# Optimization experiments

Measured on AMD Instinct MI355X. Metric: run time of the kernel, lower is better.

The kernel has to match this reference:

```python
import jax, jax.numpy as jnp
import numpy as np

N_NODES = 100000
N_EDGES = 640000
IN_DIM = 64
HID = 128
NUM_GRAPHS = 128
MPNN_STEPS = 3
S2S_STEPS = 3


def setup_inputs() -> dict:
    key = jax.random.key(0)
    ks = jax.random.split(key, 20)
    x = jax.random.normal(ks[0], (N_NODES, IN_DIM), dtype=jnp.float32)
    edge_index = jax.random.randint(ks[1], (2, N_EDGES), 0, N_NODES, dtype=jnp.int32)
    batch = jnp.sort(jax.random.randint(ks[2], (N_NODES,), 0, NUM_GRAPHS, dtype=jnp.int32))
    s = 1.0 / np.sqrt(HID)
    params = {
        # input layer Linear(64 -> 128)
        'W_in': jax.random.normal(ks[3], (HID, IN_DIM), dtype=jnp.float32) * s,
        'b_in': jax.random.normal(ks[4], (HID,), dtype=jnp.float32) * s,
        # MGU parameters (torch.randn init in source)
        'W_f': jax.random.normal(ks[5], (HID, HID), dtype=jnp.float32),
        'U_f': jax.random.normal(ks[6], (HID, HID), dtype=jnp.float32),
        'b_f': jax.random.normal(ks[7], (HID,), dtype=jnp.float32),
        'W_h': jax.random.normal(ks[8], (HID, HID), dtype=jnp.float32),
        'U_h': jax.random.normal(ks[9], (HID, HID), dtype=jnp.float32),
        'b_h': jax.random.normal(ks[10], (HID,), dtype=jnp.float32),
        # Set2Set LSTM: input 2*HID, hidden HID, gate order i,f,g,o
        'lstm_w_ih': jax.random.normal(ks[11], (4 * HID, 2 * HID), dtype=jnp.float32) * s,
        'lstm_w_hh': jax.random.normal(ks[12], (4 * HID, HID), dtype=jnp.float32) * s,
        'lstm_b_ih': jax.random.normal(ks[13], (4 * HID,), dtype=jnp.float32) * s,
        'lstm_b_hh': jax.random.normal(ks[14], (4 * HID,), dtype=jnp.float32) * s,
        # prediction layer Linear(2*HID -> 1)
        'W_pred': jax.random.normal(ks[15], (1, 2 * HID), dtype=jnp.float32) * s,
        'b_pred': jax.random.normal(ks[16], (1,), dtype=jnp.float32) * s,
    }
    return {'x': x, 'edge_index': edge_index, 'batch': batch, **params}


def _mpnn_mgu(h, src, dst, W_f, U_f, b_f, W_h, U_h, b_h):
    # sum-aggregate neighbor messages: m_i = sum_{j->i} h_j
    m = jax.ops.segment_sum(h[src], dst, num_segments=N_NODES)  # [N, H]
    f_t = jax.nn.sigmoid(m @ W_f.T + h @ U_f.T + b_f)
    h_hat = jnp.tanh(m @ W_h.T + (f_t * h) @ U_h.T + b_h)
    return (1.0 - f_t) * h + f_t * h_hat


def _set2set(x, batch, w_ih, w_hh, b_ih, b_hh):
    G, H = NUM_GRAPHS, HID
    q_star = jnp.zeros((G, 2 * H), dtype=x.dtype)
    h_l = jnp.zeros((G, H), dtype=x.dtype)
    c_l = jnp.zeros((G, H), dtype=x.dtype)
    for _ in range(S2S_STEPS):
        gates = q_star @ w_ih.T + h_l @ w_hh.T + b_ih + b_hh  # [G, 4H]
        i, f, g, o = jnp.split(gates, 4, axis=-1)
        c_l = jax.nn.sigmoid(f) * c_l + jax.nn.sigmoid(i) * jnp.tanh(g)
        h_l = jax.nn.sigmoid(o) * jnp.tanh(c_l)
        q = h_l  # [G, H]
        # attention over nodes within each graph segment
        e = jnp.sum(x * q[batch], axis=-1)  # [N]
        e_max = jax.ops.segment_max(e, batch, num_segments=G)
        a_un = jnp.exp(e - e_max[batch])
        denom = jax.ops.segment_sum(a_un, batch, num_segments=G)
        a = a_un / denom[batch]
        r = jax.ops.segment_sum(a[:, None] * x, batch, num_segments=G)  # [G, H]
        q_star = jnp.concatenate([q, r], axis=-1)
    return q_star


def reference(x, edge_index, batch, W_in, b_in, W_f, U_f, b_f, W_h, U_h, b_h,
              lstm_w_ih, lstm_w_hh, lstm_b_ih, lstm_b_hh, W_pred, b_pred):
    h = jax.nn.relu(x @ W_in.T + b_in)  # [N, HID]
    src, dst = edge_index[0], edge_index[1]
    for _ in range(MPNN_STEPS):
        h = _mpnn_mgu(h, src, dst, W_f, U_f, b_f, W_h, U_h, b_h)
    q_star = _set2set(h, batch, lstm_w_ih, lstm_w_hh, lstm_b_ih, lstm_b_hh)  # [G, 2H]
    return q_star @ W_pred.T + b_pred  # [G, 1]
```

## Files before the change

### kernel.cpp

```cpp
#include <hip/hip_runtime.h>
#include <math.h>

#define N_NODES 100000
#define N_EDGES 640000
#define IN_DIM 64
#define HID 128
#define NGRAPH 128

typedef __bf16 bf16x2 __attribute__((ext_vector_type(2)));
typedef __bf16 bf16x4 __attribute__((ext_vector_type(4)));
typedef __bf16 bf16x8 __attribute__((ext_vector_type(8)));
typedef float f32x4 __attribute__((ext_vector_type(4)));

#define LDST 136

__device__ __forceinline__ float sigmoid_f(float z) {
  return __fdividef(1.f, 1.f + __expf(-z));
}
__device__ __forceinline__ float tanh_f(float z) {
  return 1.f - __fdividef(2.f, __expf(2.f * z) + 1.f);
}

__device__ __forceinline__ void fma44(const float4 A[4], const float4 B[4], float acc[4][4]) {
#pragma unroll
  for (int i2 = 0; i2 < 4; ++i2) {
    acc[i2][0] += A[i2].x*B[0].x + A[i2].y*B[1].x + A[i2].z*B[2].x + A[i2].w*B[3].x;
    acc[i2][1] += A[i2].x*B[0].y + A[i2].y*B[1].y + A[i2].z*B[2].y + A[i2].w*B[3].y;
    acc[i2][2] += A[i2].x*B[0].z + A[i2].y*B[1].z + A[i2].z*B[2].z + A[i2].w*B[3].z;
    acc[i2][3] += A[i2].x*B[0].w + A[i2].y*B[1].w + A[i2].z*B[2].w + A[i2].w*B[3].w;
  }
}

__global__ __launch_bounds__(256) void k_input(const float* __restrict__ x,
                                               const float* __restrict__ W,
                                               const float* __restrict__ b,
                                               float* __restrict__ h) {
  __shared__ float wS[64][132];
  __shared__ float xS[32][68];
  int t = threadIdx.x;
  int nb = blockIdx.x * 32;
#pragma unroll
  for (int i = 0; i < 8; ++i) {
    int idx4 = i * 256 + t;
    int j = idx4 >> 4, kq = idx4 & 15;
    float4 v = ((const float4*)W)[j * 16 + kq];
    wS[4*kq+0][j] = v.x; wS[4*kq+1][j] = v.y; wS[4*kq+2][j] = v.z; wS[4*kq+3][j] = v.w;
  }
#pragma unroll
  for (int i = 0; i < 2; ++i) {
    int idx4 = i * 256 + t;
    int n = idx4 >> 4, kq = idx4 & 15;
    float4 v = ((const float4*)x)[(nb + n) * 16 + kq];
    *((float4*)&xS[n][4*kq]) = v;
  }
  __syncthreads();
  int bq = t & 31, a = t >> 5;
  float acc[4][4] = {};
#pragma unroll
  for (int kk4 = 0; kk4 < 16; ++kk4) {
    float4 A[4], B[4];
#pragma unroll
    for (int i2 = 0; i2 < 4; ++i2) A[i2] = *((const float4*)&xS[4*a+i2][4*kk4]);
#pragma unroll
    for (int c = 0; c < 4; ++c) B[c] = *((const float4*)&wS[4*kk4+c][4*bq]);
    fma44(A, B, acc);
  }
  float4 bb = ((const float4*)b)[bq];
  float ba[4] = {bb.x, bb.y, bb.z, bb.w};
#pragma unroll
  for (int i2 = 0; i2 < 4; ++i2) {
    float4 o;
    o.x = fmaxf(acc[i2][0] + ba[0], 0.f);
    o.y = fmaxf(acc[i2][1] + ba[1], 0.f);
    o.z = fmaxf(acc[i2][2] + ba[2], 0.f);
    o.w = fmaxf(acc[i2][3] + ba[3], 0.f);
    ((float4*)h)[(nb + 4*a + i2) * 32 + bq] = o;
  }
}

__global__ __launch_bounds__(256) void k_hist(const int* __restrict__ dst,
                                              int* __restrict__ deg) {
  int e = blockIdx.x * 256 + threadIdx.x;
  if (e < N_EDGES) atomicAdd(&deg[dst[e]], 1);
}

#define SCAN_CHUNK 4096
#define SCAN_NB 25

__global__ __launch_bounds__(256) void k_scan_part(const int* __restrict__ deg,
                                                   int* __restrict__ bsum) {
  __shared__ int red[256];
  int t = threadIdx.x, b = blockIdx.x;
  int base = b * SCAN_CHUNK + t * 16;
  int s = 0;
#pragma unroll
  for (int i = 0; i < 16; ++i) {
    int idx = base + i;
    if (idx < N_NODES) s += deg[idx];
  }
  red[t] = s;
  __syncthreads();
  for (int off = 128; off > 0; off >>= 1) {
    if (t < off) red[t] += red[t + off];
    __syncthreads();
  }
  if (t == 0) bsum[b] = red[0];
}

__global__ void k_scan_mid(const int* __restrict__ bsum, int* __restrict__ boff,
                           int* __restrict__ rowstart) {
  if (threadIdx.x == 0) {
    int run = 0;
    for (int i = 0; i < SCAN_NB; ++i) { boff[i] = run; run += bsum[i]; }
    rowstart[N_NODES] = run;
  }
}

__global__ __launch_bounds__(256) void k_scan_final(const int* __restrict__ deg,
                                                    const int* __restrict__ boff,
                                                    int* __restrict__ rowstart) {
  __shared__ int ts[256];
  int t = threadIdx.x, b = blockIdx.x;
  int base = b * SCAN_CHUNK + t * 16;
  int v[16];
  int s = 0;
#pragma unroll
  for (int i = 0; i < 16; ++i) {
    int idx = base + i;
    v[i] = (idx < N_NODES) ? deg[idx] : 0;
    s += v[i];
  }
  ts[t] = s;
  __syncthreads();
  for (int off = 1; off < 256; off <<= 1) {
    int add = (t >= off) ? ts[t - off] : 0;
    __syncthreads();
    ts[t] += add;
    __syncthreads();
  }
  int run = boff[b] + ts[t] - s;
#pragma unroll
  for (int i = 0; i < 16; ++i) {
    int idx = base + i;
    if (idx < N_NODES) rowstart[idx] = run;
    run += v[i];
  }
}

__global__ __launch_bounds__(256) void k_fill(const int* __restrict__ src,
                                              const int* __restrict__ dst,
                                              int* __restrict__ cursor,
                                              int* __restrict__ srcSorted) {
  int e = blockIdx.x * 256 + threadIdx.x;
  if (e >= N_EDGES) return;
  int d = dst[e];
  int p = atomicAdd(&cursor[d], 1);
  srcSorted[p] = src[e];
}

__global__ __launch_bounds__(256) void k_wsplit(const float* __restrict__ W0,
                                                const float* __restrict__ W1,
                                                const float* __restrict__ W2,
                                                const float* __restrict__ W3,
                                                __bf16* __restrict__ Whi,
                                                __bf16* __restrict__ Wlo) {
  int id = blockIdx.x * 256 + threadIdx.x;
  int mat = id >> 14, idx = id & 16383;
  const float* W = (mat == 0) ? W0 : (mat == 1) ? W1 : (mat == 2) ? W2 : W3;
  float v = W[idx];
  __bf16 hi = (__bf16)v;
  Whi[id] = hi;
  Wlo[id] = (__bf16)(v - (float)hi);
}

__global__ __launch_bounds__(256) void k_gather(const float* __restrict__ h,
                                                const int* __restrict__ rowstart,
                                                const int* __restrict__ srcSorted,
                                                float* __restrict__ m) {
  int node = blockIdx.x * 8 + (threadIdx.x >> 5);
  if (node >= N_NODES) return;
  int li = threadIdx.x & 31;
  int j0 = rowstart[node], j1 = rowstart[node + 1];
  const float4* h4 = (const float4*)h;
  float4 a0 = {0.f, 0.f, 0.f, 0.f}, a1 = {0.f, 0.f, 0.f, 0.f};
  int j = j0;
  for (; j + 1 < j1; j += 2) {
    int s0 = srcSorted[j], s1 = srcSorted[j + 1];
    float4 v0 = h4[s0 * 32 + li];
    float4 v1 = h4[s1 * 32 + li];
    a0.x += v0.x; a0.y += v0.y; a0.z += v0.z; a0.w += v0.w;
    a1.x += v1.x; a1.y += v1.y; a1.z += v1.z; a1.w += v1.w;
  }
  if (j < j1) {
    int s0 = srcSorted[j];
    float4 v0 = h4[s0 * 32 + li];
    a0.x += v0.x; a0.y += v0.y; a0.z += v0.z; a0.w += v0.w;
  }
  float4 o = {a0.x + a1.x, a0.y + a1.y, a0.z + a1.z, a0.w + a1.w};
  ((float4*)m)[node * 32 + li] = o;
}

__global__ __launch_bounds__(256) void k_mgu(float* __restrict__ h,
                                             const float* __restrict__ m,
                                             const __bf16* __restrict__ Whi,
                                             const __bf16* __restrict__ Wlo,
                                             const float* __restrict__ bfp,
                                             const float* __restrict__ bhp) {
  __shared__ __bf16 mHi[64 * LDST], mLo[64 * LDST];
  __shared__ __bf16 hHi[64 * LDST], hLo[64 * LDST];
  const int t = threadIdx.x;
  const int nb = blockIdx.x * 64;

#pragma unroll
  for (int i = 0; i < 8; ++i) {
    int idx4 = i * 256 + t;
    int n = idx4 >> 5, kq = idx4 & 31;
    float4 vm = ((const float4*)m)[(nb + n) * 32 + kq];
    float4 vh = ((const float4*)h)[(nb + n) * 32 + kq];
    bf16x4 mh, ml, hh, hl;
    mh[0] = (__bf16)vm.x; ml[0] = (__bf16)(vm.x - (float)mh[0]);
    mh[1] = (__bf16)vm.y; ml[1] = (__bf16)(vm.y - (float)mh[1]);
    mh[2] = (__bf16)vm.z; ml[2] = (__bf16)(vm.z - (float)mh[2]);
    mh[3] = (__bf16)vm.w; ml[3] = (__bf16)(vm.w - (float)mh[3]);
    hh[0] = (__bf16)vh.x; hl[0] = (__bf16)(vh.x - (float)hh[0]);
    hh[1] = (__bf16)vh.y; hl[1] = (__bf16)(vh.y - (float)hh[1]);
    hh[2] = (__bf16)vh.z; hl[2] = (__bf16)(vh.z - (float)hh[2]);
    hh[3] = (__bf16)vh.w; hl[3] = (__bf16)(vh.w - (float)hh[3]);
    int e0 = n * LDST + 4 * kq;
    *(bf16x4*)&mHi[e0] = mh; *(bf16x4*)&mLo[e0] = ml;
    *(bf16x4*)&hHi[e0] = hh; *(bf16x4*)&hLo[e0] = hl;
  }
  __syncthreads();

  const int w = t >> 6, l = t & 63;
  const int lj = l & 15, q = l >> 4;

  float bfj[2], bhj[2];
#pragma unroll
  for (int ct = 0; ct < 2; ++ct) {
    int j = (2 * w + ct) * 16 + lj;
    bfj[ct] = bfp[j];
    bhj[ct] = bhp[j];
  }

  f32x4 acc[4][2] = {};

#pragma unroll
  for (int kc = 0; kc < 128; kc += 32) {
    bf16x8 bwh[2], bwl[2], buh[2], bul[2];
#pragma unroll
    for (int ct = 0; ct < 2; ++ct) {
      int off = ((2 * w + ct) * 16 + lj) * 128 + kc + q * 8;
      bwh[ct] = *(const bf16x8*)&Whi[off];
      bwl[ct] = *(const bf16x8*)&Wlo[off];
      buh[ct] = *(const bf16x8*)&Whi[16384 + off];
      bul[ct] = *(const bf16x8*)&Wlo[16384 + off];
    }
#pragma unroll
    for (int rt = 0; rt < 4; ++rt) {
      int e0 = (rt * 16 + lj) * LDST + kc + q * 8;
      bf16x8 amh = *(const bf16x8*)&mHi[e0];
      bf16x8 aml = *(const bf16x8*)&mLo[e0];
      bf16x8 ahh = *(const bf16x8*)&hHi[e0];
      bf16x8 ahl = *(const bf16x8*)&hLo[e0];
#pragma unroll
      for (int ct = 0; ct < 2; ++ct) {
        f32x4 a = acc[rt][ct];
        a = __builtin_amdgcn_mfma_f32_16x16x32_bf16(amh, bwh[ct], a, 0, 0, 0);
        a = __builtin_amdgcn_mfma_f32_16x16x32_bf16(amh, bwl[ct], a, 0, 0, 0);
        a = __builtin_amdgcn_mfma_f32_16x16x32_bf16(aml, bwh[ct], a, 0, 0, 0);
        a = __builtin_amdgcn_mfma_f32_16x16x32_bf16(ahh, buh[ct], a, 0, 0, 0);
        a = __builtin_amdgcn_mfma_f32_16x16x32_bf16(ahh, bul[ct], a, 0, 0, 0);
        a = __builtin_amdgcn_mfma_f32_16x16x32_bf16(ahl, buh[ct], a, 0, 0, 0);
        acc[rt][ct] = a;
      }
    }
  }

  __syncthreads();
  float fv[4][2][4], hvv[4][2][4];
#pragma unroll
  for (int rt = 0; rt < 4; ++rt)
#pragma unroll
    for (int ct = 0; ct < 2; ++ct) {
      int j = (2 * w + ct) * 16 + lj;
#pragma unroll
      for (int r = 0; r < 4; ++r) {
        int nl = rt * 16 + q * 4 + r;
        float z = acc[rt][ct][r] + bfj[ct];
        float f = sigmoid_f(z);
        int he = nl * LDST + j;
        float hval = (float)hHi[he] + (float)hLo[he];
        float g = f * hval;
        __bf16 ghi = (__bf16)g;
        hHi[he] = ghi;
        hLo[he] = (__bf16)(g - (float)ghi);
        fv[rt][ct][r] = f;
        hvv[rt][ct][r] = hval;
        acc[rt][ct][r] = 0.f;
      }
    }
  __syncthreads();

#pragma unroll
  for (int kc = 0; kc < 128; kc += 32) {
    bf16x8 bwh[2], bwl[2], buh[2], bul[2];
#pragma unroll
    for (int ct = 0; ct < 2; ++ct) {
      int off = ((2 * w + ct) * 16 + lj) * 128 + kc + q * 8;
      bwh[ct] = *(const bf16x8*)&Whi[2 * 16384 + off];
      bwl[ct] = *(const bf16x8*)&Wlo[2 * 16384 + off];
      buh[ct] = *(const bf16x8*)&Whi[3 * 16384 + off];
      bul[ct] = *(const bf16x8*)&Wlo[3 * 16384 + off];
    }
#pragma unroll
    for (int rt = 0; rt < 4; ++rt) {
      int e0 = (rt * 16 + lj) * LDST + kc + q * 8;
      bf16x8 amh = *(const bf16x8*)&mHi[e0];
      bf16x8 aml = *(const bf16x8*)&mLo[e0];
      bf16x8 agh = *(const bf16x8*)&hHi[e0];
      bf16x8 agl = *(const bf16x8*)&hLo[e0];
#pragma unroll
      for (int ct = 0; ct < 2; ++ct) {
        f32x4 a = acc[rt][ct];
        a = __builtin_amdgcn_mfma_f32_16x16x32_bf16(amh, bwh[ct], a, 0, 0, 0);
        a = __builtin_amdgcn_mfma_f32_16x16x32_bf16(amh, bwl[ct], a, 0, 0, 0);
        a = __builtin_amdgcn_mfma_f32_16x16x32_bf16(aml, bwh[ct], a, 0, 0, 0);
        a = __builtin_amdgcn_mfma_f32_16x16x32_bf16(agh, buh[ct], a, 0, 0, 0);
        a = __builtin_amdgcn_mfma_f32_16x16x32_bf16(agh, bul[ct], a, 0, 0, 0);
        a = __builtin_amdgcn_mfma_f32_16x16x32_bf16(agl, buh[ct], a, 0, 0, 0);
        acc[rt][ct] = a;
      }
    }
  }

#pragma unroll
  for (int rt = 0; rt < 4; ++rt)
#pragma unroll
    for (int ct = 0; ct < 2; ++ct) {
      int j = (2 * w + ct) * 16 + lj;
#pragma unroll
      for (int r = 0; r < 4; ++r) {
        float T = tanh_f(acc[rt][ct][r] + bhj[ct]);
        float f = fv[rt][ct][r];
        float hn = (1.f - f) * hvv[rt][ct][r] + f * T;
        h[(nb + rt * 16 + q * 4 + r) * 128 + j] = hn;
      }
    }
}

__global__ __launch_bounds__(1024) void k_s2s(const float* __restrict__ h,
                                              const int* __restrict__ batch,
                                              const float* __restrict__ w_ih,
                                              const float* __restrict__ w_hh,
                                              const float* __restrict__ b_ih,
                                              const float* __restrict__ b_hh,
                                              const float* __restrict__ Wp,
                                              const float* __restrict__ bp,
                                              float* __restrict__ out) {
  const int g = blockIdx.x, t = threadIdx.x;
  const int w = t >> 6, l = t & 63;
  const int half = l >> 5, li = l & 31;
  const int hw = 2 * w + half;
  __shared__ float qs[256];
  __shared__ float hl[128], cl[128];
  __shared__ float gates[512];
  __shared__ float redM[32], redS[32], scl[32];
  __shared__ float rPart[32][132];
  __shared__ float gInvS;
  __shared__ int bnd[2];

  if (t < 2) {
    int tgt = g + t;
    int lo = 0, hi = N_NODES;
    while (lo < hi) { int mid = (lo + hi) >> 1; if (batch[mid] < tgt) lo = mid + 1; else hi = mid; }
    bnd[t] = lo;
  }
  if (t < 256) qs[t] = 0.f;
  if (t < 128) { hl[t] = 0.f; cl[t] = 0.f; }
  __syncthreads();
  const int s0 = bnd[0], s1 = bnd[1];

  for (int step = 0; step < 3; ++step) {
#pragma unroll 2
    for (int jt = w; jt < 512; jt += 16) {
      const float* wi = w_ih + jt * 256;
      const float* wh = w_hh + jt * 128;
      float s = qs[l] * wi[l] + qs[l+64] * wi[l+64]
              + qs[l+128] * wi[l+128] + qs[l+192] * wi[l+192]
              + hl[l] * wh[l] + hl[l+64] * wh[l+64];
#pragma unroll
      for (int o = 32; o > 0; o >>= 1) s += __shfl_xor(s, o, 64);
      if (l == 0) gates[jt] = s + b_ih[jt] + b_hh[jt];
    }
    __syncthreads();
    if (t < 128) {
      float gi = gates[t], gf = gates[128 + t], gg = gates[256 + t], go = gates[384 + t];
      float c = sigmoid_f(gf) * cl[t] + sigmoid_f(gi) * tanh_f(gg);
      float hh = sigmoid_f(go) * tanh_f(c);
      cl[t] = c;
      hl[t] = hh;
      qs[t] = hh;
    }
    __syncthreads();

    float mw = -INFINITY, sw = 0.f;
    float4 racc = {0.f, 0.f, 0.f, 0.f};
    const float4* h4 = (const float4*)h;
    const float q0 = qs[4*li], q1 = qs[4*li+1], q2 = qs[4*li+2], q3 = qs[4*li+3];
    int n = s0 + hw;
    for (; n + 32 < s1; n += 64) {
      float4 hv0 = h4[n * 32 + li];
      float4 hv1 = h4[(n + 32) * 32 + li];
      float v0 = hv0.x * q0 + hv0.y * q1 + hv0.z * q2 + hv0.w * q3;
      float v1 = hv1.x * q0 + hv1.y * q1 + hv1.z * q2 + hv1.w * q3;
#pragma unroll
      for (int o = 16; o > 0; o >>= 1) {
        v0 += __shfl_xor(v0, o, 64);
        v1 += __shfl_xor(v1, o, 64);
      }
      float nm = fmaxf(mw, fmaxf(v0, v1));
      float sc = __expf(mw - nm);
      float w0 = __expf(v0 - nm);
      float w1 = __expf(v1 - nm);
      sw = sw * sc + w0 + w1;
      racc.x = racc.x * sc + w0 * hv0.x + w1 * hv1.x;
      racc.y = racc.y * sc + w0 * hv0.y + w1 * hv1.y;
      racc.z = racc.z * sc + w0 * hv0.z + w1 * hv1.z;
      racc.w = racc.w * sc + w0 * hv0.w + w1 * hv1.w;
      mw = nm;
    }
    for (; n < s1; n += 32) {
      float4 hv = h4[n * 32 + li];
      float v = hv.x * q0 + hv.y * q1 + hv.z * q2 + hv.w * q3;
#pragma unroll
      for (int o = 16; o > 0; o >>= 1) v += __shfl_xor(v, o, 64);
      float nm = fmaxf(mw, v);
      float sc = __expf(mw - nm);
      float wg = __expf(v - nm);
      sw = sw * sc + wg;
      racc.x = racc.x * sc + wg * hv.x;
      racc.y = racc.y * sc + wg * hv.y;
      racc.z = racc.z * sc + wg * hv.z;
      racc.w = racc.w * sc + wg * hv.w;
      mw = nm;
    }
    if (li == 0) { redM[hw] = mw; redS[hw] = sw; }
    *(float4*)&rPart[hw][4 * li] = racc;
    __syncthreads();
    if (t == 0) {
      float M = -INFINITY;
      for (int i = 0; i < 32; ++i) M = fmaxf(M, redM[i]);
      float S = 0.f;
      for (int i = 0; i < 32; ++i) {
        float s_ = (redM[i] > -INFINITY && M > -INFINITY) ? __expf(redM[i] - M) : 0.f;
        scl[i] = s_;
        S += redS[i] * s_;
      }
      gInvS = (S > 0.f) ? __fdividef(1.f, S) : 0.f;
    }
    __syncthreads();
    if (t < 128) {
      float inv = gInvS;
      float r = 0.f;
#pragma unroll
      for (int i = 0; i < 32; ++i) r += rPart[i][t] * scl[i];
      qs[128 + t] = r * inv;
    }
    __syncthreads();
  }

  __shared__ float pr[256];
  if (t < 256) pr[t] = qs[t] * Wp[t];
  __syncthreads();
  if (t < 128) pr[t] += pr[t + 128];
  __syncthreads();
  if (t < 64) {
    float s = pr[t] + pr[t + 64];
#pragma unroll
    for (int o = 32; o > 0; o >>= 1) s += __shfl_xor(s, o, 64);
    if (t == 0) out[g] = s + bp[0];
  }
}

extern "C" void kernel_launch(void* const* d_in, const int* in_sizes, int n_in,
                              void* d_out, int out_size, void* d_ws, size_t ws_size,
                              hipStream_t stream) {
  const float* x      = (const float*)d_in[0];
  const int*   ei     = (const int*)d_in[1];
  const int*   batch  = (const int*)d_in[2];
  const float* W_in   = (const float*)d_in[3];
  const float* b_in   = (const float*)d_in[4];
  const float* W_f    = (const float*)d_in[5];
  const float* U_f    = (const float*)d_in[6];
  const float* b_f    = (const float*)d_in[7];
  const float* W_h    = (const float*)d_in[8];
  const float* U_h    = (const float*)d_in[9];
  const float* b_h    = (const float*)d_in[10];
  const float* w_ih   = (const float*)d_in[11];
  const float* w_hh   = (const float*)d_in[12];
  const float* b_ih   = (const float*)d_in[13];
  const float* b_hh   = (const float*)d_in[14];
  const float* W_pred = (const float*)d_in[15];
  const float* b_pred = (const float*)d_in[16];
  float* out = (float*)d_out;

  char* ws = (char*)d_ws;
  float* h      = (float*)(ws);
  float* m      = (float*)(ws + 51200000);
  int*   rowstart = (int*)(ws + 103063808);
  int*   srcSorted= (int*)(ws + 103463824);
  int*   bsum   = (int*)  (ws + 106023824);
  int*   boff   = (int*)  (ws + 106023936);
  int*    deg    = (int*)(ws + 102400000);
  int*    cursor = (int*)(ws + 102400000);
  __bf16* Whi    = (__bf16*)(ws + 102400000);
  __bf16* Wlo    = (__bf16*)(ws + 102531072);

  const int* src = ei;
  const int* dst = ei + N_EDGES;

  hipMemsetAsync(deg, 0, N_NODES * 4, stream);
  k_hist<<<(N_EDGES + 255) / 256, 256, 0, stream>>>(dst, deg);
  k_scan_part<<<SCAN_NB, 256, 0, stream>>>(deg, bsum);
  k_scan_mid<<<1, 32, 0, stream>>>(bsum, boff, rowstart);
  k_scan_final<<<SCAN_NB, 256, 0, stream>>>(deg, boff, rowstart);
  hipMemcpyAsync(cursor, rowstart, N_NODES * 4, hipMemcpyDeviceToDevice, stream);
  k_fill<<<(N_EDGES + 255) / 256, 256, 0, stream>>>(src, dst, cursor, srcSorted);

  k_wsplit<<<256, 256, 0, stream>>>(W_f, U_f, W_h, U_h, Whi, Wlo);

  k_input<<<N_NODES / 32, 256, 0, stream>>>(x, W_in, b_in, h);

  for (int step = 0; step < 3; ++step) {
    k_gather<<<(N_NODES + 7) / 8, 256, 0, stream>>>(h, rowstart, srcSorted, m);
    k_mgu<<<(N_NODES + 63) / 64, 256, 0, stream>>>(h, m, Whi, Wlo, b_f, b_h);
  }

  k_s2s<<<NGRAPH, 1024, 0, stream>>>(h, batch, w_ih, w_hh, b_ih, b_hh,
                                     W_pred, b_pred, out);
}
```

Before: 725.1 us.

## Fuse neighbor gather into MGU kernel with ping-pong hidden buffers

```diff
diff --git a/kernel.cpp b/kernel.cpp
--- a/kernel.cpp
+++ b/kernel.cpp
@@ -173,35 +173,10 @@
   Wlo[id] = (__bf16)(v - (float)hi);
 }
 
-__global__ __launch_bounds__(256) void k_gather(const float* __restrict__ h,
-                                                const int* __restrict__ rowstart,
-                                                const int* __restrict__ srcSorted,
-                                                float* __restrict__ m) {
-  int node = blockIdx.x * 8 + (threadIdx.x >> 5);
-  if (node >= N_NODES) return;
-  int li = threadIdx.x & 31;
-  int j0 = rowstart[node], j1 = rowstart[node + 1];
-  const float4* h4 = (const float4*)h;
-  float4 a0 = {0.f, 0.f, 0.f, 0.f}, a1 = {0.f, 0.f, 0.f, 0.f};
-  int j = j0;
-  for (; j + 1 < j1; j += 2) {
-    int s0 = srcSorted[j], s1 = srcSorted[j + 1];
-    float4 v0 = h4[s0 * 32 + li];
-    float4 v1 = h4[s1 * 32 + li];
-    a0.x += v0.x; a0.y += v0.y; a0.z += v0.z; a0.w += v0.w;
-    a1.x += v1.x; a1.y += v1.y; a1.z += v1.z; a1.w += v1.w;
-  }
-  if (j < j1) {
-    int s0 = srcSorted[j];
-    float4 v0 = h4[s0 * 32 + li];
-    a0.x += v0.x; a0.y += v0.y; a0.z += v0.z; a0.w += v0.w;
-  }
-  float4 o = {a0.x + a1.x, a0.y + a1.y, a0.z + a1.z, a0.w + a1.w};
-  ((float4*)m)[node * 32 + li] = o;
-}
-
-__global__ __launch_bounds__(256) void k_mgu(float* __restrict__ h,
-                                             const float* __restrict__ m,
+__global__ __launch_bounds__(256) void k_mgu(float* __restrict__ hdst,
+                                             const float* __restrict__ hsrc,
+                                             const int* __restrict__ rowstart,
+                                             const int* __restrict__ srcSorted,
                                              const __bf16* __restrict__ Whi,
                                              const __bf16* __restrict__ Wlo,
                                              const float* __restrict__ bfp,
@@ -215,20 +190,48 @@
   for (int i = 0; i < 8; ++i) {
     int idx4 = i * 256 + t;
     int n = idx4 >> 5, kq = idx4 & 31;
-    float4 vm = ((const float4*)m)[(nb + n) * 32 + kq];
-    float4 vh = ((const float4*)h)[(nb + n) * 32 + kq];
-    bf16x4 mh, ml, hh, hl;
-    mh[0] = (__bf16)vm.x; ml[0] = (__bf16)(vm.x - (float)mh[0]);
-    mh[1] = (__bf16)vm.y; ml[1] = (__bf16)(vm.y - (float)mh[1]);
-    mh[2] = (__bf16)vm.z; ml[2] = (__bf16)(vm.z - (float)mh[2]);
-    mh[3] = (__bf16)vm.w; ml[3] = (__bf16)(vm.w - (float)mh[3]);
+    float4 vh = ((const float4*)hsrc)[(nb + n) * 32 + kq];
+    bf16x4 hh, hl;
     hh[0] = (__bf16)vh.x; hl[0] = (__bf16)(vh.x - (float)hh[0]);
     hh[1] = (__bf16)vh.y; hl[1] = (__bf16)(vh.y - (float)hh[1]);
     hh[2] = (__bf16)vh.z; hl[2] = (__bf16)(vh.z - (float)hh[2]);
     hh[3] = (__bf16)vh.w; hl[3] = (__bf16)(vh.w - (float)hh[3]);
     int e0 = n * LDST + 4 * kq;
-    *(bf16x4*)&mHi[e0] = mh; *(bf16x4*)&mLo[e0] = ml;
     *(bf16x4*)&hHi[e0] = hh; *(bf16x4*)&hLo[e0] = hl;
+  }
+
+  {
+    const int grp = t >> 5, li = t & 31;
+    const float4* h4 = (const float4*)hsrc;
+#pragma unroll 1
+    for (int c = 0; c < 8; ++c) {
+      int nl = c * 8 + grp;
+      int node = nb + nl;
+      int j0 = 0, j1 = 0;
+      if (node < N_NODES) { j0 = rowstart[node]; j1 = rowstart[node + 1]; }
+      float4 a0 = {0.f, 0.f, 0.f, 0.f}, a1 = {0.f, 0.f, 0.f, 0.f};
+      int j = j0;
+      for (; j + 1 < j1; j += 2) {
+        int s0 = srcSorted[j], s1 = srcSorted[j + 1];
+        float4 v0 = h4[s0 * 32 + li];
+        float4 v1 = h4[s1 * 32 + li];
+        a0.x += v0.x; a0.y += v0.y; a0.z += v0.z; a0.w += v0.w;
+        a1.x += v1.x; a1.y += v1.y; a1.z += v1.z; a1.w += v1.w;
+      }
+      if (j < j1) {
+        int s0 = srcSorted[j];
+        float4 v0 = h4[s0 * 32 + li];
+        a0.x += v0.x; a0.y += v0.y; a0.z += v0.z; a0.w += v0.w;
+      }
+      float4 o = {a0.x + a1.x, a0.y + a1.y, a0.z + a1.z, a0.w + a1.w};
+      bf16x4 mh, ml;
+      mh[0] = (__bf16)o.x; ml[0] = (__bf16)(o.x - (float)mh[0]);
+      mh[1] = (__bf16)o.y; ml[1] = (__bf16)(o.y - (float)mh[1]);
+      mh[2] = (__bf16)o.z; ml[2] = (__bf16)(o.z - (float)mh[2]);
+      mh[3] = (__bf16)o.w; ml[3] = (__bf16)(o.w - (float)mh[3]);
+      int e0 = nl * LDST + 4 * li;
+      *(bf16x4*)&mHi[e0] = mh; *(bf16x4*)&mLo[e0] = ml;
+    }
   }
   __syncthreads();
 
@@ -341,10 +344,11 @@
       int j = (2 * w + ct) * 16 + lj;
 #pragma unroll
       for (int r = 0; r < 4; ++r) {
+        int node = nb + rt * 16 + q * 4 + r;
         float T = tanh_f(acc[rt][ct][r] + bhj[ct]);
         float f = fv[rt][ct][r];
         float hn = (1.f - f) * hvv[rt][ct][r] + f * T;
-        h[(nb + rt * 16 + q * 4 + r) * 128 + j] = hn;
+        if (node < N_NODES) hdst[node * 128 + j] = hn;
       }
     }
 }
@@ -506,8 +510,8 @@
   float* out = (float*)d_out;
 
   char* ws = (char*)d_ws;
-  float* h      = (float*)(ws);
-  float* m      = (float*)(ws + 51200000);
+  float* h0     = (float*)(ws);
+  float* h1     = (float*)(ws + 51200000);
   int*   rowstart = (int*)(ws + 103063808);
   int*   srcSorted= (int*)(ws + 103463824);
   int*   bsum   = (int*)  (ws + 106023824);
@@ -530,13 +534,13 @@
 
   k_wsplit<<<256, 256, 0, stream>>>(W_f, U_f, W_h, U_h, Whi, Wlo);
 
-  k_input<<<N_NODES / 32, 256, 0, stream>>>(x, W_in, b_in, h);
-
-  for (int step = 0; step < 3; ++step) {
-    k_gather<<<(N_NODES + 7) / 8, 256, 0, stream>>>(h, rowstart, srcSorted, m);
-    k_mgu<<<(N_NODES + 63) / 64, 256, 0, stream>>>(h, m, Whi, Wlo, b_f, b_h);
-  }
-
-  k_s2s<<<NGRAPH, 1024, 0, stream>>>(h, batch, w_ih, w_hh, b_ih, b_hh,
+  k_input<<<N_NODES / 32, 256, 0, stream>>>(x, W_in, b_in, h0);
+
+  const int NBLK = (N_NODES + 63) / 64;
+  k_mgu<<<NBLK, 256, 0, stream>>>(h1, h0, rowstart, srcSorted, Whi, Wlo, b_f, b_h);
+  k_mgu<<<NBLK, 256, 0, stream>>>(h0, h1, rowstart, srcSorted, Whi, Wlo, b_f, b_h);
+  k_mgu<<<NBLK, 256, 0, stream>>>(h1, h0, rowstart, srcSorted, Whi, Wlo, b_f, b_h);
+
+  k_s2s<<<NGRAPH, 1024, 0, stream>>>(h1, batch, w_ih, w_hh, b_ih, b_hh,
                                      W_pred, b_pred, out);
 }
```

After: 839.0 us. 1.16x slower.

## Split Set2Set attention across four blocks per graph with last-block LSTM update

Applied to the files above, without the earlier changes.

```diff
diff --git a/kernel.cpp b/kernel.cpp
--- a/kernel.cpp
+++ b/kernel.cpp
@@ -6,6 +6,8 @@
 #define IN_DIM 64
 #define HID 128
 #define NGRAPH 128
+#define SPLIT 4
+#define PSTR 132
 
 typedef __bf16 bf16x2 __attribute__((ext_vector_type(2)));
 typedef __bf16 bf16x4 __attribute__((ext_vector_type(4)));
@@ -349,26 +351,50 @@
     }
 }
 
-__global__ __launch_bounds__(1024) void k_s2s(const float* __restrict__ h,
-                                              const int* __restrict__ batch,
-                                              const float* __restrict__ w_ih,
-                                              const float* __restrict__ w_hh,
-                                              const float* __restrict__ b_ih,
-                                              const float* __restrict__ b_hh,
-                                              const float* __restrict__ Wp,
-                                              const float* __restrict__ bp,
-                                              float* __restrict__ out) {
-  const int g = blockIdx.x, t = threadIdx.x;
+__global__ __launch_bounds__(128) void k_s2s_init(const float* __restrict__ b_ih,
+                                                  const float* __restrict__ b_hh,
+                                                  float* __restrict__ q_buf,
+                                                  float* __restrict__ hc_buf,
+                                                  int* __restrict__ done) {
+  int g = blockIdx.x, t = threadIdx.x;
+  float gi = b_ih[t] + b_hh[t];
+  float gf = b_ih[128 + t] + b_hh[128 + t];
+  float gg = b_ih[256 + t] + b_hh[256 + t];
+  float go = b_ih[384 + t] + b_hh[384 + t];
+  (void)gf;
+  float c = sigmoid_f(gi) * tanh_f(gg);
+  float hh = sigmoid_f(go) * tanh_f(c);
+  q_buf[g * 128 + t] = hh;
+  hc_buf[g * 256 + t] = hh;
+  hc_buf[g * 256 + 128 + t] = c;
+  if (t < 3) done[t * NGRAPH + g] = 0;
+}
+
+__global__ __launch_bounds__(1024, 8) void k_s2s_step(const float* __restrict__ h,
+                                                      const int* __restrict__ batch,
+                                                      float* __restrict__ q_buf,
+                                                      float* __restrict__ hc_buf,
+                                                      float* __restrict__ partials,
+                                                      int* __restrict__ done,
+                                                      const float* __restrict__ w_ih,
+                                                      const float* __restrict__ w_hh,
+                                                      const float* __restrict__ b_ih,
+                                                      const float* __restrict__ b_hh,
+                                                      const float* __restrict__ Wp,
+                                                      const float* __restrict__ bp,
+                                                      float* __restrict__ out,
+                                                      int step) {
+  const int b = blockIdx.x;
+  const int g = b >> 2, p = b & (SPLIT - 1);
+  const int t = threadIdx.x;
   const int w = t >> 6, l = t & 63;
   const int half = l >> 5, li = l & 31;
   const int hw = 2 * w + half;
-  __shared__ float qs[256];
-  __shared__ float hl[128], cl[128];
-  __shared__ float gates[512];
   __shared__ float redM[32], redS[32], scl[32];
   __shared__ float rPart[32][132];
-  __shared__ float gInvS;
+  __shared__ float sMS[2];
   __shared__ int bnd[2];
+  __shared__ int amLast;
 
   if (t < 2) {
     int tgt = g + t;
@@ -376,110 +402,167 @@
     while (lo < hi) { int mid = (lo + hi) >> 1; if (batch[mid] < tgt) lo = mid + 1; else hi = mid; }
     bnd[t] = lo;
   }
-  if (t < 256) qs[t] = 0.f;
-  if (t < 128) { hl[t] = 0.f; cl[t] = 0.f; }
   __syncthreads();
   const int s0 = bnd[0], s1 = bnd[1];
-
-  for (int step = 0; step < 3; ++step) {
-#pragma unroll 2
-    for (int jt = w; jt < 512; jt += 16) {
-      const float* wi = w_ih + jt * 256;
-      const float* wh = w_hh + jt * 128;
-      float s = qs[l] * wi[l] + qs[l+64] * wi[l+64]
-              + qs[l+128] * wi[l+128] + qs[l+192] * wi[l+192]
-              + hl[l] * wh[l] + hl[l+64] * wh[l+64];
+  const int len = s1 - s0;
+  const int ps = s0 + (len * p) / SPLIT;
+  const int pe = s0 + (len * (p + 1)) / SPLIT;
+
+  float4 qv = ((const float4*)(q_buf + g * 128))[li];
+  const float q0 = qv.x, q1 = qv.y, q2 = qv.z, q3 = qv.w;
+
+  float mw = -INFINITY, sw = 0.f;
+  float4 racc = {0.f, 0.f, 0.f, 0.f};
+  const float4* h4 = (const float4*)h;
+  int n = ps + hw;
+  for (; n + 32 < pe; n += 64) {
+    float4 hv0 = h4[n * 32 + li];
+    float4 hv1 = h4[(n + 32) * 32 + li];
+    float v0 = hv0.x * q0 + hv0.y * q1 + hv0.z * q2 + hv0.w * q3;
+    float v1 = hv1.x * q0 + hv1.y * q1 + hv1.z * q2 + hv1.w * q3;
+#pragma unroll
+    for (int o = 16; o > 0; o >>= 1) {
+      v0 += __shfl_xor(v0, o, 64);
+      v1 += __shfl_xor(v1, o, 64);
+    }
+    float nm = fmaxf(mw, fmaxf(v0, v1));
+    float sc = __expf(mw - nm);
+    float w0 = __expf(v0 - nm);
+    float w1 = __expf(v1 - nm);
+    sw = sw * sc + w0 + w1;
+    racc.x = racc.x * sc + w0 * hv0.x + w1 * hv1.x;
+    racc.y = racc.y * sc + w0 * hv0.y + w1 * hv1.y;
+    racc.z = racc.z * sc + w0 * hv0.z + w1 * hv1.z;
+    racc.w = racc.w * sc + w0 * hv0.w + w1 * hv1.w;
+    mw = nm;
+  }
+  for (; n < pe; n += 32) {
+    float4 hv = h4[n * 32 + li];
+    float v = hv.x * q0 + hv.y * q1 + hv.z * q2 + hv.w * q3;
+#pragma unroll
+    for (int o = 16; o > 0; o >>= 1) v += __shfl_xor(v, o, 64);
+    float nm = fmaxf(mw, v);
+    float sc = __expf(mw - nm);
+    float wg = __expf(v - nm);
+    sw = sw * sc + wg;
+    racc.x = racc.x * sc + wg * hv.x;
+    racc.y = racc.y * sc + wg * hv.y;
+    racc.z = racc.z * sc + wg * hv.z;
+    racc.w = racc.w * sc + wg * hv.w;
+    mw = nm;
+  }
+  if (li == 0) { redM[hw] = mw; redS[hw] = sw; }
+  *(float4*)&rPart[hw][4 * li] = racc;
+  __syncthreads();
+  if (t == 0) {
+    float M = -INFINITY;
+    for (int i = 0; i < 32; ++i) M = fmaxf(M, redM[i]);
+    float S = 0.f;
+    for (int i = 0; i < 32; ++i) {
+      float s_ = (redM[i] > -INFINITY && M > -INFINITY) ? __expf(redM[i] - M) : 0.f;
+      scl[i] = s_;
+      S += redS[i] * s_;
+    }
+    sMS[0] = M; sMS[1] = S;
+  }
+  __syncthreads();
+  float* P = partials + (g * SPLIT + p) * PSTR;
+  if (t == 0) { P[0] = sMS[0]; P[1] = sMS[1]; }
+  if (t < 128) {
+    float r = 0.f;
+#pragma unroll
+    for (int i = 0; i < 32; ++i) r += rPart[i][t] * scl[i];
+    P[4 + t] = r;
+  }
+
+  __syncthreads();
+  if (t == 0) {
+    __threadfence();
+    int old = atomicAdd(&done[step * NGRAPH + g], 1);
+    amLast = (old == 3);
+  }
+  __syncthreads();
+  if (!amLast) return;
+  if (t == 0) __threadfence();
+  __syncthreads();
+
+  __shared__ float sc2[SPLIT];
+  __shared__ float qstar[256];
+  __shared__ float hcl[256];
+  __shared__ float gates[512];
+  __shared__ float invS_sh;
+  const float* PP = partials + g * SPLIT * PSTR;
+
+  if (t == 0) {
+    float M = -INFINITY;
+#pragma unroll
+    for (int pp = 0; pp < SPLIT; ++pp) M = fmaxf(M, PP[pp * PSTR]);
+    float S = 0.f;
+#pragma unroll
+    for (int pp = 0; pp < SPLIT; ++pp) {
+      float mp = PP[pp * PSTR];
+      float s_ = (mp > -INFINITY && M > -INFINITY) ? __expf(mp - M) : 0.f;
+      sc2[pp] = s_;
+      S += PP[pp * PSTR + 1] * s_;
+    }
+    invS_sh = (S > 0.f) ? __fdividef(1.f, S) : 0.f;
+  }
+  if (t < 128) {
+    qstar[t] = q_buf[g * 128 + t];
+    hcl[t] = hc_buf[g * 256 + t];
+    hcl[128 + t] = hc_buf[g * 256 + 128 + t];
+  }
+  __syncthreads();
+  if (t < 128) {
+    float r = 0.f;
+#pragma unroll
+    for (int pp = 0; pp < SPLIT; ++pp) r += PP[pp * PSTR + 4 + t] * sc2[pp];
+    qstar[128 + t] = r * invS_sh;
+  }
+  __syncthreads();
+
+  if (step == 2) {
+    __shared__ float pr[256];
+    if (t < 256) pr[t] = qstar[t] * Wp[t];
+    __syncthreads();
+    if (t < 128) pr[t] += pr[t + 128];
+    __syncthreads();
+    if (t < 64) {
+      float s = pr[t] + pr[t + 64];
 #pragma unroll
       for (int o = 32; o > 0; o >>= 1) s += __shfl_xor(s, o, 64);
-      if (l == 0) gates[jt] = s + b_ih[jt] + b_hh[jt];
-    }
-    __syncthreads();
-    if (t < 128) {
-      float gi = gates[t], gf = gates[128 + t], gg = gates[256 + t], go = gates[384 + t];
-      float c = sigmoid_f(gf) * cl[t] + sigmoid_f(gi) * tanh_f(gg);
-      float hh = sigmoid_f(go) * tanh_f(c);
-      cl[t] = c;
-      hl[t] = hh;
-      qs[t] = hh;
-    }
-    __syncthreads();
-
-    float mw = -INFINITY, sw = 0.f;
-    float4 racc = {0.f, 0.f, 0.f, 0.f};
-    const float4* h4 = (const float4*)h;
-    const float q0 = qs[4*li], q1 = qs[4*li+1], q2 = qs[4*li+2], q3 = qs[4*li+3];
-    int n = s0 + hw;
-    for (; n + 32 < s1; n += 64) {
-      float4 hv0 = h4[n * 32 + li];
-      float4 hv1 = h4[(n + 32) * 32 + li];
-      float v0 = hv0.x * q0 + hv0.y * q1 + hv0.z * q2 + hv0.w * q3;
-      float v1 = hv1.x * q0 + hv1.y * q1 + hv1.z * q2 + hv1.w * q3;
-#pragma unroll
-      for (int o = 16; o > 0; o >>= 1) {
-        v0 += __shfl_xor(v0, o, 64);
-        v1 += __shfl_xor(v1, o, 64);
-      }
-      float nm = fmaxf(mw, fmaxf(v0, v1));
-      float sc = __expf(mw - nm);
-      float w0 = __expf(v0 - nm);
-      float w1 = __expf(v1 - nm);
-      sw = sw * sc + w0 + w1;
-      racc.x = racc.x * sc + w0 * hv0.x + w1 * hv1.x;
-      racc.y = racc.y * sc + w0 * hv0.y + w1 * hv1.y;
-      racc.z = racc.z * sc + w0 * hv0.z + w1 * hv1.z;
-      racc.w = racc.w * sc + w0 * hv0.w + w1 * hv1.w;
-      mw = nm;
-    }
-    for (; n < s1; n += 32) {
-      float4 hv = h4[n * 32 + li];
-      float v = hv.x * q0 + hv.y * q1 + hv.z * q2 + hv.w * q3;
-#pragma unroll
-      for (int o = 16; o > 0; o >>= 1) v += __shfl_xor(v, o, 64);
-      float nm = fmaxf(mw, v);
-      float sc = __expf(mw - nm);
-      float wg = __expf(v - nm);
-      sw = sw * sc + wg;
-      racc.x = racc.x * sc + wg * hv.x;
-      racc.y = racc.y * sc + wg * hv.y;
-      racc.z = racc.z * sc + wg * hv.z;
-      racc.w = racc.w * sc + wg * hv.w;
-      mw = nm;
-    }
-    if (li == 0) { redM[hw] = mw; redS[hw] = sw; }
-    *(float4*)&rPart[hw][4 * li] = racc;
-    __syncthreads();
-    if (t == 0) {
-      float M = -INFINITY;
-      for (int i = 0; i < 32; ++i) M = fmaxf(M, redM[i]);
-      float S = 0.f;
-      for (int i = 0; i < 32; ++i) {
-        float s_ = (redM[i] > -INFINITY && M > -INFINITY) ? __expf(redM[i] - M) : 0.f;
-        scl[i] = s_;
-        S += redS[i] * s_;
-      }
-      gInvS = (S > 0.f) ? __fdividef(1.f, S) : 0.f;
-    }
-    __syncthreads();
-    if (t < 128) {
-      float inv = gInvS;
-      float r = 0.f;
-#pragma unroll
-      for (int i = 0; i < 32; ++i) r += rPart[i][t] * scl[i];
-      qs[128 + t] = r * inv;
-    }
-    __syncthreads();
-  }
-
-  __shared__ float pr[256];
-  if (t < 256) pr[t] = qs[t] * Wp[t];
-  __syncthreads();
-  if (t < 128) pr[t] += pr[t + 128];
-  __syncthreads();
-  if (t < 64) {
-    float s = pr[t] + pr[t + 64];
-#pragma unroll
-    for (int o = 32; o > 0; o >>= 1) s += __shfl_xor(s, o, 64);
-    if (t == 0) out[g] = s + bp[0];
+      if (t == 0) out[g] = s + bp[0];
+    }
+    return;
+  }
+
+  if (t < 512) {
+    int j = t;
+    const float4* wi4 = (const float4*)(w_ih + j * 256);
+    const float4* wh4 = (const float4*)(w_hh + j * 128);
+    float s = 0.f;
+#pragma unroll 8
+    for (int k = 0; k < 64; ++k) {
+      float4 a = wi4[k];
+      float4 bb = *(const float4*)&qstar[4 * k];
+      s += a.x * bb.x + a.y * bb.y + a.z * bb.z + a.w * bb.w;
+    }
+#pragma unroll 8
+    for (int k = 0; k < 32; ++k) {
+      float4 a = wh4[k];
+      float4 bb = *(const float4*)&hcl[4 * k];
+      s += a.x * bb.x + a.y * bb.y + a.z * bb.z + a.w * bb.w;
+    }
+    gates[j] = s + b_ih[j] + b_hh[j];
+  }
+  __syncthreads();
+  if (t < 128) {
+    float gi = gates[t], gf = gates[128 + t], gg = gates[256 + t], go = gates[384 + t];
+    float c = sigmoid_f(gf) * hcl[128 + t] + sigmoid_f(gi) * tanh_f(gg);
+    float hh = sigmoid_f(go) * tanh_f(c);
+    hc_buf[g * 256 + t] = hh;
+    hc_buf[g * 256 + 128 + t] = c;
+    q_buf[g * 128 + t] = hh;
   }
 }
 
@@ -516,6 +599,10 @@
   int*    cursor = (int*)(ws + 102400000);
   __bf16* Whi    = (__bf16*)(ws + 102400000);
   __bf16* Wlo    = (__bf16*)(ws + 102531072);
+  float* q_buf    = (float*)(ws + 51200000);
+  float* hc_buf   = (float*)(ws + 51200000 + 65536);
+  float* partials = (float*)(ws + 51200000 + 196608);
+  int*   done     = (int*)  (ws + 51200000 + 466944);
 
   const int* src = ei;
   const int* dst = ei + N_EDGES;
@@ -537,6 +624,11 @@
     k_mgu<<<(N_NODES + 63) / 64, 256, 0, stream>>>(h, m, Whi, Wlo, b_f, b_h);
   }
 
-  k_s2s<<<NGRAPH, 1024, 0, stream>>>(h, batch, w_ih, w_hh, b_ih, b_hh,
-                                     W_pred, b_pred, out);
-}
+  k_s2s_init<<<NGRAPH, 128, 0, stream>>>(b_ih, b_hh, q_buf, hc_buf, done);
+  for (int step = 0; step < 3; ++step) {
+    k_s2s_step<<<NGRAPH * SPLIT, 1024, 0, stream>>>(h, batch, q_buf, hc_buf,
+                                                    partials, done,
+                                                    w_ih, w_hh, b_ih, b_hh,
+                                                    W_pred, b_pred, out, step);
+  }
+}
```

Result: slower. 797.2 us (+9.9%).
